# Performance work log

Measured on AMD Instinct MI355X. Metric: run time of the kernel, lower is better.

The kernel has to match this reference:

```python
import jax, jax.numpy as jnp
import numpy as np

NEG_INF = -1e30


def setup_inputs() -> dict:
    key = jax.random.key(0)
    kq, kk, kv, ks = jax.random.split(key, 4)
    B, H, S, D = 2, 16, 2048, 64
    return {
        "q": jax.random.normal(kq, (B, H, S, D), dtype=jnp.float32),
        "k": jax.random.normal(kk, (B, H, S, D), dtype=jnp.float32),
        "v": jax.random.normal(kv, (B, H, S, D), dtype=jnp.float32),
        "sink_weights": jax.random.normal(ks, (H,), dtype=jnp.float32),
        "sliding_window": 1024,
    }


def reference(q, k, v, sink_weights, sliding_window):
    """Sliding-window causal attention with a learnable attention-sink logit.

    Equivalent to FlexAttention.forward with sink_weights given: an extra kv
    position (the sink) is appended whose score is replaced by sink_weights[h]
    and whose value is zero -> it only adds mass to the softmax denominator.
    """
    B, H, S_q, D = q.shape
    S_kv = k.shape[2]
    scale = 1.0 / np.sqrt(D)

    # [B, H, S_q, S_kv] raw scores
    scores = jnp.einsum("bhqd,bhkd->bhqk", q, k) * scale

    q_idx = jnp.arange(S_q)[:, None]
    kv_idx = jnp.arange(S_kv)[None, :]
    keep = (kv_idx <= q_idx) & (q_idx - kv_idx <= sliding_window)  # [S_q, S_kv]
    scores = jnp.where(keep[None, None], scores, NEG_INF)

    # sink column: per-head learnable logit, always visible
    sink_col = jnp.broadcast_to(
        sink_weights[None, :, None, None], (B, H, S_q, 1)
    )
    logits = jnp.concatenate([scores, sink_col], axis=-1)  # [B,H,S_q,S_kv+1]

    probs = jax.nn.softmax(logits, axis=-1)
    # sink value is zero, so only the first S_kv prob columns hit v
    out = jnp.einsum("bhqk,bhkd->bhqd", probs[..., :S_kv], v)
    return out
```

## Files before the change

kernel.cpp:

```cpp
#include <hip/hip_runtime.h>


typedef __bf16 bf16x8 __attribute__((ext_vector_type(8)));
typedef __bf16 bf16x4 __attribute__((ext_vector_type(4)));
typedef float  f32x16 __attribute__((ext_vector_type(16)));

#define SK 72
#define SV 72
#define SPP 72
#define NT 256
#define NEG_BIG (-3.0e38f)

__device__ const int SEG_N[24] = {3,2,2,2,2,1,2,1, 1,1,1,1,1,1,1,1, 1,1,1,1,1,1,1,1};
__device__ const int SEG_IT[24][3] = {
  {0,1,2},{2,3,0},{3,4,0},{4,5,0},{5,6,0},{6,0,0},{6,7,0},{7,0,0},
  {8,0,0},{8,0,0},{9,0,0},{9,0,0},{10,0,0},{10,0,0},{11,0,0},{11,0,0},
  {12,0,0},{12,0,0},{13,0,0},{13,0,0},{14,0,0},{14,0,0},{15,0,0},{15,0,0}};
__device__ const int SEG_J0[24][3] = {
  {0,0,0},{3,0,0},{6,0,0},{7,0,0},{6,0,0},{3,0,0},{12,0,0},{7,0,0},
  {0,0,0},{9,0,0},{0,0,0},{9,0,0},{0,0,0},{9,0,0},{0,0,0},{9,0,0},
  {0,0,0},{9,0,0},{0,0,0},{9,0,0},{0,0,0},{9,0,0},{0,0,0},{9,0,0}};
__device__ const int SEG_J1[24][3] = {
  {2,4,3},{6,6,0},{8,7,0},{10,6,0},{12,3,0},{12,0,0},{14,7,0},{16,0,0},
  {9,0,0},{18,0,0},{9,0,0},{18,0,0},{9,0,0},{18,0,0},{9,0,0},{18,0,0},
  {9,0,0},{18,0,0},{9,0,0},{18,0,0},{9,0,0},{18,0,0},{9,0,0},{18,0,0}};
__device__ const int SEG_SX[24][3] = {
  {0,0,0},{1,0,0},{1,0,0},{1,0,0},{1,0,0},{1,0,0},{2,0,0},{1,0,0},
  {0,0,0},{1,0,0},{0,0,0},{1,0,0},{0,0,0},{1,0,0},{0,0,0},{1,0,0},
  {0,0,0},{1,0,0},{0,0,0},{1,0,0},{0,0,0},{1,0,0},{0,0,0},{1,0,0}};
__device__ const int NSEG_ITEM[16] = {1,1,2,2,2,2,3,2, 2,2,2,2,2,2,2,2};

__global__ __launch_bounds__(NT, 3) void flex_r5_main(
    const float* __restrict__ Q, const float* __restrict__ K,
    const float* __restrict__ V, const float* __restrict__ SINKW,
    const int* __restrict__ SWIN, void* __restrict__ WS,
    const int H, const int S)
{
    const int t    = threadIdx.x;
    const int lane = t & 63;
    const int w    = t >> 6;
    const int c    = lane & 31;
    const int hl   = lane >> 5;
    const int W    = SWIN[0];
    const float scale = 0.125f;

    const int NBH = gridDim.x / 24;
    const int bh  = blockIdx.x / 24;
    const int b24 = blockIdx.x - bh * 24;
    const int h   = bh % H;
    const float sw = SINKW[h];

    __shared__ __align__(16) __bf16 k_lds[64 * SK];
    __shared__ __align__(16) __bf16 v_lds[64 * SV];
    __shared__ __align__(16) __bf16 p_lds[4 * 32 * SPP];

    const size_t basebh = (size_t)bh * S * 64;
    const float4* kp4 = (const float4*)(K + basebh);
    const float4* vp4 = (const float4*)(V + basebh);
    __bf16* O_ws = (__bf16*)WS;
    float2* ml_ws = (float2*)((char*)WS + (size_t)NBH * 48 * 16384);

    const int dgi = t & 15;
    const int kgi = t >> 4;
    float4 kreg[4], vreg[4];

    const int ns = SEG_N[b24];

    {
        const int it0 = SEG_IT[b24][0];
        const int ktA0 = (2 * it0 - 16 > 0) ? (2 * it0 - 16) : 0;
        const int kt = ktA0 + SEG_J0[b24][0];
        #pragma unroll
        for (int i = 0; i < 4; ++i) kreg[i] = kp4[kt * 1024 + i * NT + t];
        #pragma unroll
        for (int kk = 0; kk < 4; ++kk) vreg[kk] = vp4[kt * 1024 + (4 * kgi + kk) * 16 + dgi];
    }

    for (int s = 0; s < ns; ++s) {
        const int item = SEG_IT[b24][s];
        const int j0   = SEG_J0[b24][s];
        const int j1   = SEG_J1[b24][s];
        const int sidx = SEG_SX[b24][s];
        const int ktA  = (2 * item - 16 > 0) ? (2 * item - 16) : 0;
        const int qw0  = item * 128 + 32 * w;
        const int qi   = qw0 + c;

        bf16x8 bq[4];
        {
            const float4* qp4 = (const float4*)(Q + basebh + (size_t)qi * 64);
            #pragma unroll
            for (int ks = 0; ks < 4; ++ks) {
                float4 f0 = qp4[4 * ks + 2 * hl];
                float4 f1 = qp4[4 * ks + 2 * hl + 1];
                bq[ks][0] = (__bf16)(f0.x * scale); bq[ks][1] = (__bf16)(f0.y * scale);
                bq[ks][2] = (__bf16)(f0.z * scale); bq[ks][3] = (__bf16)(f0.w * scale);
                bq[ks][4] = (__bf16)(f1.x * scale); bq[ks][5] = (__bf16)(f1.y * scale);
                bq[ks][6] = (__bf16)(f1.z * scale); bq[ks][7] = (__bf16)(f1.w * scale);
            }
        }

        float mrun = (sidx == 0) ? sw : NEG_BIG;
        float lrun = (sidx == 0) ? 1.0f : 0.0f;
        f32x16 accO0, accO1;
        #pragma unroll
        for (int i = 0; i < 16; ++i) { accO0[i] = 0.0f; accO1[i] = 0.0f; }

        for (int j = j0; j < j1; ++j) {
            const int k0 = (ktA + j) * 64;
            __syncthreads();

            #pragma unroll
            for (int i = 0; i < 4; ++i) {
                const int flat = i * NT + t;
                const int key = flat >> 4, dd = flat & 15;
                float4 f = kreg[i];
                bf16x4 b = { (__bf16)f.x, (__bf16)f.y, (__bf16)f.z, (__bf16)f.w };
                *(bf16x4*)&k_lds[key * SK + 4 * dd] = b;
            }
            {
                float4 a0 = vreg[0], a1 = vreg[1], a2 = vreg[2], a3 = vreg[3];
                bf16x4 w0 = { (__bf16)a0.x, (__bf16)a1.x, (__bf16)a2.x, (__bf16)a3.x };
                bf16x4 w1 = { (__bf16)a0.y, (__bf16)a1.y, (__bf16)a2.y, (__bf16)a3.y };
                bf16x4 w2 = { (__bf16)a0.z, (__bf16)a1.z, (__bf16)a2.z, (__bf16)a3.z };
                bf16x4 w3 = { (__bf16)a0.w, (__bf16)a1.w, (__bf16)a2.w, (__bf16)a3.w };
                *(bf16x4*)&v_lds[(4 * dgi + 0) * SV + 4 * kgi] = w0;
                *(bf16x4*)&v_lds[(4 * dgi + 1) * SV + 4 * kgi] = w1;
                *(bf16x4*)&v_lds[(4 * dgi + 2) * SV + 4 * kgi] = w2;
                *(bf16x4*)&v_lds[(4 * dgi + 3) * SV + 4 * kgi] = w3;
            }
            int nkt = -1;
            if (j + 1 < j1) nkt = ktA + j + 1;
            else if (s + 1 < ns) {
                const int it2 = SEG_IT[b24][s + 1];
                const int ktA2 = (2 * it2 - 16 > 0) ? (2 * it2 - 16) : 0;
                nkt = ktA2 + SEG_J0[b24][s + 1];
            }
            if (nkt >= 0) {
                #pragma unroll
                for (int i = 0; i < 4; ++i) kreg[i] = kp4[nkt * 1024 + i * NT + t];
                #pragma unroll
                for (int kk = 0; kk < 4; ++kk) vreg[kk] = vp4[nkt * 1024 + (4 * kgi + kk) * 16 + dgi];
            }
            __syncthreads();

            f32x16 accS0, accS1;
            #pragma unroll
            for (int i = 0; i < 16; ++i) { accS0[i] = 0.0f; accS1[i] = 0.0f; }
            #pragma unroll
            for (int ks = 0; ks < 4; ++ks) {
                bf16x8 ka0 = *(const bf16x8*)&k_lds[c * SK + 16 * ks + 8 * hl];
                bf16x8 ka1 = *(const bf16x8*)&k_lds[(32 + c) * SK + 16 * ks + 8 * hl];
                accS0 = __builtin_amdgcn_mfma_f32_32x32x16_bf16(ka0, bq[ks], accS0, 0, 0, 0);
                accS1 = __builtin_amdgcn_mfma_f32_32x32x16_bf16(ka1, bq[ks], accS1, 0, 0, 0);
            }

            const bool interior = (k0 + 63 <= qw0) && (qw0 + 31 - k0 <= W);
            if (!interior) {
                #pragma unroll
                for (int rg = 0; rg < 16; ++rg) {
                    const int kb  = (rg & 3) + 8 * (rg >> 2) + 4 * hl;
                    const int ki0 = k0 + kb, ki1 = k0 + 32 + kb;
                    if (!((ki0 <= qi) && (qi - ki0 <= W))) accS0[rg] = -1e30f;
                    if (!((ki1 <= qi) && (qi - ki1 <= W))) accS1[rg] = -1e30f;
                }
            }

            float mx = accS0[0];
            #pragma unroll
            for (int i = 1; i < 16; ++i) mx = fmaxf(mx, accS0[i]);
            #pragma unroll
            for (int i = 0; i < 16; ++i) mx = fmaxf(mx, accS1[i]);
            mx = fmaxf(mx, __shfl_xor(mx, 32, 64));
            const float mnew  = fmaxf(mrun, mx);
            const float alpha = __expf(mrun - mnew);
            float ps = 0.0f;
            #pragma unroll
            for (int i = 0; i < 16; ++i) { float p = __expf(accS0[i] - mnew); accS0[i] = p; ps += p; }
            #pragma unroll
            for (int i = 0; i < 16; ++i) { float p = __expf(accS1[i] - mnew); accS1[i] = p; ps += p; }
            ps += __shfl_xor(ps, 32, 64);
            lrun = lrun * alpha + ps;
            mrun = mnew;
            #pragma unroll
            for (int i = 0; i < 16; ++i) { accO0[i] *= alpha; accO1[i] *= alpha; }

            __bf16* pw = p_lds + w * 32 * SPP;
            #pragma unroll
            for (int rg = 0; rg < 4; ++rg) {
                bf16x4 b0 = { (__bf16)accS0[4*rg+0], (__bf16)accS0[4*rg+1],
                              (__bf16)accS0[4*rg+2], (__bf16)accS0[4*rg+3] };
                bf16x4 b1 = { (__bf16)accS1[4*rg+0], (__bf16)accS1[4*rg+1],
                              (__bf16)accS1[4*rg+2], (__bf16)accS1[4*rg+3] };
                *(bf16x4*)&pw[c * SPP +      8 * rg + 4 * hl] = b0;
                *(bf16x4*)&pw[c * SPP + 32 + 8 * rg + 4 * hl] = b1;
            }

            #pragma unroll
            for (int ks = 0; ks < 4; ++ks) {
                bf16x8 bp  = *(const bf16x8*)&pw[c * SPP + 16 * ks + 8 * hl];
                bf16x8 va0 = *(const bf16x8*)&v_lds[c * SV + 16 * ks + 8 * hl];
                bf16x8 va1 = *(const bf16x8*)&v_lds[(32 + c) * SV + 16 * ks + 8 * hl];
                accO0 = __builtin_amdgcn_mfma_f32_32x32x16_bf16(va0, bp, accO0, 0, 0, 0);
                accO1 = __builtin_amdgcn_mfma_f32_32x32x16_bf16(va1, bp, accO1, 0, 0, 0);
            }
        }

        const int slot = (bh * 16 + item) * 3 + sidx;
        const int qrel = 32 * w + c;
        if (hl == 0) ml_ws[(size_t)slot * 128 + qrel] = make_float2(mrun, lrun);
        __bf16* Os = O_ws + (size_t)slot * 8192 + (size_t)qrel * 64;
        #pragma unroll
        for (int qd = 0; qd < 4; ++qd) {
            const int d0 = 8 * qd + 4 * hl;
            bf16x4 b0 = { (__bf16)accO0[4*qd+0], (__bf16)accO0[4*qd+1],
                          (__bf16)accO0[4*qd+2], (__bf16)accO0[4*qd+3] };
            bf16x4 b1 = { (__bf16)accO1[4*qd+0], (__bf16)accO1[4*qd+1],
                          (__bf16)accO1[4*qd+2], (__bf16)accO1[4*qd+3] };
            *(bf16x4*)&Os[d0]      = b0;
            *(bf16x4*)&Os[32 + d0] = b1;
        }
    }
}

__global__ __launch_bounds__(256) void flex_r5_combine(
    const void* __restrict__ WS, float* __restrict__ OUT, const int H, const int S)
{
    const int NBH  = gridDim.x / 16;
    const int bi   = blockIdx.x;
    const int bh   = bi >> 4;
    const int item = bi & 15;
    const int ns   = NSEG_ITEM[item];
    const int t    = threadIdx.x;
    const int q    = t >> 1;
    const int half = t & 1;

    const __bf16* O_ws = (const __bf16*)WS;
    const float2* ml_ws = (const float2*)((const char*)WS + (size_t)NBH * 48 * 16384);
    const int base = bi * 3;

    float m[3], lv[3], a[3];
    float mst = NEG_BIG;
    for (int s = 0; s < ns; ++s) {
        float2 e = ml_ws[(size_t)(base + s) * 128 + q];
        m[s] = e.x; lv[s] = e.y;
        mst = fmaxf(mst, m[s]);
    }
    float lst = 0.0f;
    for (int s = 0; s < ns; ++s) { a[s] = __expf(m[s] - mst); lst += a[s] * lv[s]; }
    const float inv = 1.0f / lst;

    float acc[32];
    #pragma unroll
    for (int i = 0; i < 32; ++i) acc[i] = 0.0f;
    for (int s = 0; s < ns; ++s) {
        const __bf16* Os = O_ws + (size_t)(base + s) * 8192 + (size_t)q * 64 + 32 * half;
        const float as = a[s];
        #pragma unroll
        for (int v8 = 0; v8 < 4; ++v8) {
            bf16x8 o = *(const bf16x8*)&Os[8 * v8];
            #pragma unroll
            for (int j = 0; j < 8; ++j) acc[8 * v8 + j] += as * (float)o[j];
        }
    }

    float* dst = OUT + (size_t)bh * S * 64 + (size_t)(item * 128 + q) * 64 + 32 * half;
    #pragma unroll
    for (int v4 = 0; v4 < 8; ++v4) {
        float4 f = { acc[4*v4+0] * inv, acc[4*v4+1] * inv,
                     acc[4*v4+2] * inv, acc[4*v4+3] * inv };
        *(float4*)&dst[4 * v4] = f;
    }
}

extern "C" void kernel_launch(void* const* d_in, const int* in_sizes, int n_in,
                              void* d_out, int out_size, void* d_ws, size_t ws_size,
                              hipStream_t stream) {
    const float* q     = (const float*)d_in[0];
    const float* k     = (const float*)d_in[1];
    const float* v     = (const float*)d_in[2];
    const float* sinkw = (const float*)d_in[3];
    const int*   swin  = (const int*)d_in[4];
    float* out = (float*)d_out;

    const int H = in_sizes[3];
    const int S = 2048;
    const int B = in_sizes[0] / (H * S * 64);
    const int NBH = B * H;


    flex_r5_main<<<dim3(NBH * 24), NT, 0, stream>>>(q, k, v, sinkw, swin, d_ws, H, S);
    flex_r5_combine<<<dim3(NBH * 16), 256, 0, stream>>>(d_ws, out, H, S);
}
```

Measured before the change: 139.9 us.

## Double-buffer K/V in LDS with XOR swizzle and direct output for early tiles

Replaces padded LDS rows with an XOR-swizzled 64-wide layout for K, V and P tiles and double-buffers K/V so the next tile is written to the alternate buffer after the PV matmul. This removes one barrier per iteration. Query items 0 and 1, which have a single segment, now write normalized fp32 output directly instead of going through the workspace, and the combine kernel skips them. The cost is roughly double the K/V LDS footprint, which may hurt occupancy at 3 blocks per CU.

New measurement: 140.0 us. About the same (+0.1%).

```diff
diff --git a/kernel.cpp b/kernel.cpp
--- a/kernel.cpp
+++ b/kernel.cpp
@@ -5,11 +5,12 @@
 typedef __bf16 bf16x4 __attribute__((ext_vector_type(4)));
 typedef float  f32x16 __attribute__((ext_vector_type(16)));
 
-#define SK 72
-#define SV 72
-#define SPP 72
 #define NT 256
 #define NEG_BIG (-3.0e38f)
+
+__device__ __forceinline__ int swz(int row, int gran) {
+    return row * 64 + ((gran ^ ((row >> 1) & 7)) << 3);
+}
 
 __device__ const int SEG_N[24] = {3,2,2,2,2,1,2,1, 1,1,1,1,1,1,1,1, 1,1,1,1,1,1,1,1};
 __device__ const int SEG_IT[24][3] = {
@@ -30,11 +31,11 @@
   {0,0,0},{1,0,0},{0,0,0},{1,0,0},{0,0,0},{1,0,0},{0,0,0},{1,0,0}};
 __device__ const int NSEG_ITEM[16] = {1,1,2,2,2,2,3,2, 2,2,2,2,2,2,2,2};
 
-__global__ __launch_bounds__(NT, 3) void flex_r5_main(
+__global__ __launch_bounds__(NT, 3) void flex_r6_main(
     const float* __restrict__ Q, const float* __restrict__ K,
     const float* __restrict__ V, const float* __restrict__ SINKW,
     const int* __restrict__ SWIN, void* __restrict__ WS,
-    const int H, const int S)
+    float* __restrict__ OUT, const int H, const int S)
 {
     const int t    = threadIdx.x;
     const int lane = t & 63;
@@ -50,14 +51,14 @@
     const int h   = bh % H;
     const float sw = SINKW[h];
 
-    __shared__ __align__(16) __bf16 k_lds[64 * SK];
-    __shared__ __align__(16) __bf16 v_lds[64 * SV];
-    __shared__ __align__(16) __bf16 p_lds[4 * 32 * SPP];
+    __shared__ __align__(16) __bf16 k_lds[2][64 * 64];
+    __shared__ __align__(16) __bf16 v_lds[2][64 * 64];
+    __shared__ __align__(16) __bf16 p_lds[4][32 * 64];
 
     const size_t basebh = (size_t)bh * S * 64;
     const float4* kp4 = (const float4*)(K + basebh);
     const float4* vp4 = (const float4*)(V + basebh);
-    __bf16* O_ws = (__bf16*)WS;
+    __bf16* O_ws  = (__bf16*)WS;
     float2* ml_ws = (float2*)((char*)WS + (size_t)NBH * 48 * 16384);
 
     const int dgi = t & 15;
@@ -74,7 +75,29 @@
         for (int i = 0; i < 4; ++i) kreg[i] = kp4[kt * 1024 + i * NT + t];
         #pragma unroll
         for (int kk = 0; kk < 4; ++kk) vreg[kk] = vp4[kt * 1024 + (4 * kgi + kk) * 16 + dgi];
-    }
+        #pragma unroll
+        for (int i = 0; i < 4; ++i) {
+            const int flat = i * NT + t;
+            const int key = flat >> 4, dd = flat & 15;
+            float4 f = kreg[i];
+            bf16x4 b = { (__bf16)f.x, (__bf16)f.y, (__bf16)f.z, (__bf16)f.w };
+            *(bf16x4*)&k_lds[0][swz(key, dd >> 1) + (dd & 1) * 4] = b;
+        }
+        {
+            float4 a0 = vreg[0], a1 = vreg[1], a2 = vreg[2], a3 = vreg[3];
+            bf16x4 w0 = { (__bf16)a0.x, (__bf16)a1.x, (__bf16)a2.x, (__bf16)a3.x };
+            bf16x4 w1 = { (__bf16)a0.y, (__bf16)a1.y, (__bf16)a2.y, (__bf16)a3.y };
+            bf16x4 w2 = { (__bf16)a0.z, (__bf16)a1.z, (__bf16)a2.z, (__bf16)a3.z };
+            bf16x4 w3 = { (__bf16)a0.w, (__bf16)a1.w, (__bf16)a2.w, (__bf16)a3.w };
+            const int gv = kgi >> 1, ov = (kgi & 1) * 4;
+            *(bf16x4*)&v_lds[0][swz(4 * dgi + 0, gv) + ov] = w0;
+            *(bf16x4*)&v_lds[0][swz(4 * dgi + 1, gv) + ov] = w1;
+            *(bf16x4*)&v_lds[0][swz(4 * dgi + 2, gv) + ov] = w2;
+            *(bf16x4*)&v_lds[0][swz(4 * dgi + 3, gv) + ov] = w3;
+        }
+    }
+
+    int par = 0;
 
     for (int s = 0; s < ns; ++s) {
         const int item = SEG_IT[b24][s];
@@ -107,27 +130,9 @@
 
         for (int j = j0; j < j1; ++j) {
             const int k0 = (ktA + j) * 64;
+
             __syncthreads();
 
-            #pragma unroll
-            for (int i = 0; i < 4; ++i) {
-                const int flat = i * NT + t;
-                const int key = flat >> 4, dd = flat & 15;
-                float4 f = kreg[i];
-                bf16x4 b = { (__bf16)f.x, (__bf16)f.y, (__bf16)f.z, (__bf16)f.w };
-                *(bf16x4*)&k_lds[key * SK + 4 * dd] = b;
-            }
-            {
-                float4 a0 = vreg[0], a1 = vreg[1], a2 = vreg[2], a3 = vreg[3];
-                bf16x4 w0 = { (__bf16)a0.x, (__bf16)a1.x, (__bf16)a2.x, (__bf16)a3.x };
-                bf16x4 w1 = { (__bf16)a0.y, (__bf16)a1.y, (__bf16)a2.y, (__bf16)a3.y };
-                bf16x4 w2 = { (__bf16)a0.z, (__bf16)a1.z, (__bf16)a2.z, (__bf16)a3.z };
-                bf16x4 w3 = { (__bf16)a0.w, (__bf16)a1.w, (__bf16)a2.w, (__bf16)a3.w };
-                *(bf16x4*)&v_lds[(4 * dgi + 0) * SV + 4 * kgi] = w0;
-                *(bf16x4*)&v_lds[(4 * dgi + 1) * SV + 4 * kgi] = w1;
-                *(bf16x4*)&v_lds[(4 * dgi + 2) * SV + 4 * kgi] = w2;
-                *(bf16x4*)&v_lds[(4 * dgi + 3) * SV + 4 * kgi] = w3;
-            }
             int nkt = -1;
             if (j + 1 < j1) nkt = ktA + j + 1;
             else if (s + 1 < ns) {
@@ -141,15 +146,16 @@
                 #pragma unroll
                 for (int kk = 0; kk < 4; ++kk) vreg[kk] = vp4[nkt * 1024 + (4 * kgi + kk) * 16 + dgi];
             }
-            __syncthreads();
-
+
+            const __bf16* kb = k_lds[par];
+            const __bf16* vb = v_lds[par];
             f32x16 accS0, accS1;
             #pragma unroll
             for (int i = 0; i < 16; ++i) { accS0[i] = 0.0f; accS1[i] = 0.0f; }
             #pragma unroll
             for (int ks = 0; ks < 4; ++ks) {
-                bf16x8 ka0 = *(const bf16x8*)&k_lds[c * SK + 16 * ks + 8 * hl];
-                bf16x8 ka1 = *(const bf16x8*)&k_lds[(32 + c) * SK + 16 * ks + 8 * hl];
+                bf16x8 ka0 = *(const bf16x8*)&kb[swz(c,      2 * ks + hl)];
+                bf16x8 ka1 = *(const bf16x8*)&kb[swz(32 + c, 2 * ks + hl)];
                 accS0 = __builtin_amdgcn_mfma_f32_32x32x16_bf16(ka0, bq[ks], accS0, 0, 0, 0);
                 accS1 = __builtin_amdgcn_mfma_f32_32x32x16_bf16(ka1, bq[ks], accS1, 0, 0, 0);
             }
@@ -158,8 +164,8 @@
             if (!interior) {
                 #pragma unroll
                 for (int rg = 0; rg < 16; ++rg) {
-                    const int kb  = (rg & 3) + 8 * (rg >> 2) + 4 * hl;
-                    const int ki0 = k0 + kb, ki1 = k0 + 32 + kb;
+                    const int kb2 = (rg & 3) + 8 * (rg >> 2) + 4 * hl;
+                    const int ki0 = k0 + kb2, ki1 = k0 + 32 + kb2;
                     if (!((ki0 <= qi) && (qi - ki0 <= W))) accS0[rg] = -1e30f;
                     if (!((ki1 <= qi) && (qi - ki1 <= W))) accS1[rg] = -1e30f;
                 }
@@ -184,51 +190,88 @@
             #pragma unroll
             for (int i = 0; i < 16; ++i) { accO0[i] *= alpha; accO1[i] *= alpha; }
 
-            __bf16* pw = p_lds + w * 32 * SPP;
+            __bf16* pw = p_lds[w];
             #pragma unroll
             for (int rg = 0; rg < 4; ++rg) {
                 bf16x4 b0 = { (__bf16)accS0[4*rg+0], (__bf16)accS0[4*rg+1],
                               (__bf16)accS0[4*rg+2], (__bf16)accS0[4*rg+3] };
                 bf16x4 b1 = { (__bf16)accS1[4*rg+0], (__bf16)accS1[4*rg+1],
                               (__bf16)accS1[4*rg+2], (__bf16)accS1[4*rg+3] };
-                *(bf16x4*)&pw[c * SPP +      8 * rg + 4 * hl] = b0;
-                *(bf16x4*)&pw[c * SPP + 32 + 8 * rg + 4 * hl] = b1;
+                *(bf16x4*)&pw[swz(c, rg)     + 4 * hl] = b0;
+                *(bf16x4*)&pw[swz(c, rg + 4) + 4 * hl] = b1;
             }
 
             #pragma unroll
             for (int ks = 0; ks < 4; ++ks) {
-                bf16x8 bp  = *(const bf16x8*)&pw[c * SPP + 16 * ks + 8 * hl];
-                bf16x8 va0 = *(const bf16x8*)&v_lds[c * SV + 16 * ks + 8 * hl];
-                bf16x8 va1 = *(const bf16x8*)&v_lds[(32 + c) * SV + 16 * ks + 8 * hl];
+                bf16x8 bp  = *(const bf16x8*)&pw[swz(c, 2 * ks + hl)];
+                bf16x8 va0 = *(const bf16x8*)&vb[swz(c,      2 * ks + hl)];
+                bf16x8 va1 = *(const bf16x8*)&vb[swz(32 + c, 2 * ks + hl)];
                 accO0 = __builtin_amdgcn_mfma_f32_32x32x16_bf16(va0, bp, accO0, 0, 0, 0);
                 accO1 = __builtin_amdgcn_mfma_f32_32x32x16_bf16(va1, bp, accO1, 0, 0, 0);
             }
-        }
-
-        const int slot = (bh * 16 + item) * 3 + sidx;
-        const int qrel = 32 * w + c;
-        if (hl == 0) ml_ws[(size_t)slot * 128 + qrel] = make_float2(mrun, lrun);
-        __bf16* Os = O_ws + (size_t)slot * 8192 + (size_t)qrel * 64;
-        #pragma unroll
-        for (int qd = 0; qd < 4; ++qd) {
-            const int d0 = 8 * qd + 4 * hl;
-            bf16x4 b0 = { (__bf16)accO0[4*qd+0], (__bf16)accO0[4*qd+1],
-                          (__bf16)accO0[4*qd+2], (__bf16)accO0[4*qd+3] };
-            bf16x4 b1 = { (__bf16)accO1[4*qd+0], (__bf16)accO1[4*qd+1],
-                          (__bf16)accO1[4*qd+2], (__bf16)accO1[4*qd+3] };
-            *(bf16x4*)&Os[d0]      = b0;
-            *(bf16x4*)&Os[32 + d0] = b1;
+
+            if (nkt >= 0) {
+                const int np = par ^ 1;
+                #pragma unroll
+                for (int i = 0; i < 4; ++i) {
+                    const int flat = i * NT + t;
+                    const int key = flat >> 4, dd = flat & 15;
+                    float4 f = kreg[i];
+                    bf16x4 b = { (__bf16)f.x, (__bf16)f.y, (__bf16)f.z, (__bf16)f.w };
+                    *(bf16x4*)&k_lds[np][swz(key, dd >> 1) + (dd & 1) * 4] = b;
+                }
+                float4 a0 = vreg[0], a1 = vreg[1], a2 = vreg[2], a3 = vreg[3];
+                bf16x4 w0 = { (__bf16)a0.x, (__bf16)a1.x, (__bf16)a2.x, (__bf16)a3.x };
+                bf16x4 w1 = { (__bf16)a0.y, (__bf16)a1.y, (__bf16)a2.y, (__bf16)a3.y };
+                bf16x4 w2 = { (__bf16)a0.z, (__bf16)a1.z, (__bf16)a2.z, (__bf16)a3.z };
+                bf16x4 w3 = { (__bf16)a0.w, (__bf16)a1.w, (__bf16)a2.w, (__bf16)a3.w };
+                const int gv = kgi >> 1, ov = (kgi & 1) * 4;
+                *(bf16x4*)&v_lds[np][swz(4 * dgi + 0, gv) + ov] = w0;
+                *(bf16x4*)&v_lds[np][swz(4 * dgi + 1, gv) + ov] = w1;
+                *(bf16x4*)&v_lds[np][swz(4 * dgi + 2, gv) + ov] = w2;
+                *(bf16x4*)&v_lds[np][swz(4 * dgi + 3, gv) + ov] = w3;
+            }
+            par ^= 1;
+        }
+
+        if (item < 2) {
+            const float inv = 1.0f / lrun;
+            float* ob = OUT + basebh + (size_t)qi * 64;
+            #pragma unroll
+            for (int rg = 0; rg < 4; ++rg) {
+                float4 f0 = { accO0[4*rg+0]*inv, accO0[4*rg+1]*inv,
+                              accO0[4*rg+2]*inv, accO0[4*rg+3]*inv };
+                float4 f1 = { accO1[4*rg+0]*inv, accO1[4*rg+1]*inv,
+                              accO1[4*rg+2]*inv, accO1[4*rg+3]*inv };
+                *(float4*)&ob[     8 * rg + 4 * hl] = f0;
+                *(float4*)&ob[32 + 8 * rg + 4 * hl] = f1;
+            }
+        } else {
+            const int slot = (bh * 16 + item) * 3 + sidx;
+            const int qrel = 32 * w + c;
+            if (hl == 0) ml_ws[(size_t)slot * 128 + qrel] = make_float2(mrun, lrun);
+            __bf16* Os = O_ws + (size_t)slot * 8192 + (size_t)qrel * 64;
+            #pragma unroll
+            for (int qd = 0; qd < 4; ++qd) {
+                const int d0 = 8 * qd + 4 * hl;
+                bf16x4 b0 = { (__bf16)accO0[4*qd+0], (__bf16)accO0[4*qd+1],
+                              (__bf16)accO0[4*qd+2], (__bf16)accO0[4*qd+3] };
+                bf16x4 b1 = { (__bf16)accO1[4*qd+0], (__bf16)accO1[4*qd+1],
+                              (__bf16)accO1[4*qd+2], (__bf16)accO1[4*qd+3] };
+                *(bf16x4*)&Os[d0]      = b0;
+                *(bf16x4*)&Os[32 + d0] = b1;
+            }
         }
     }
 }
 
-__global__ __launch_bounds__(256) void flex_r5_combine(
+__global__ __launch_bounds__(256) void flex_r6_combine(
     const void* __restrict__ WS, float* __restrict__ OUT, const int H, const int S)
 {
-    const int NBH  = gridDim.x / 16;
+    const int NBH  = gridDim.x / 14;
     const int bi   = blockIdx.x;
-    const int bh   = bi >> 4;
-    const int item = bi & 15;
+    const int bh   = bi / 14;
+    const int item = 2 + (bi - bh * 14);
     const int ns   = NSEG_ITEM[item];
     const int t    = threadIdx.x;
     const int q    = t >> 1;
@@ -236,7 +279,7 @@
 
     const __bf16* O_ws = (const __bf16*)WS;
     const float2* ml_ws = (const float2*)((const char*)WS + (size_t)NBH * 48 * 16384);
-    const int base = bi * 3;
+    const int base = (bh * 16 + item) * 3;
 
     float m[3], lv[3], a[3];
     float mst = NEG_BIG;
@@ -287,7 +330,6 @@
     const int B = in_sizes[0] / (H * S * 64);
     const int NBH = B * H;
 
-
-    flex_r5_main<<<dim3(NBH * 24), NT, 0, stream>>>(q, k, v, sinkw, swin, d_ws, H, S);
-    flex_r5_combine<<<dim3(NBH * 16), 256, 0, stream>>>(d_ws, out, H, S);
+    flex_r6_main<<<dim3(NBH * 24), NT, 0, stream>>>(q, k, v, sinkw, swin, d_ws, out, H, S);
+    flex_r6_combine<<<dim3(NBH * 14), 256, 0, stream>>>(d_ws, out, H, S);
 }
```
